# Kernel optimization log

Measured on AMD Instinct MI355X. Metric: run time of the kernel, lower is better.

The kernel has to match this reference:

```python
import jax, jax.numpy as jnp
import numpy as np

EPS = 1e-6
BN_EPS = 1e-5


def _grid_idx(loc, Hg, Wg):
    # loc: [B, N0, 2] in [-1, 1], (x, y) order -> nearest cell index in Hg x Wg grid
    loc = jnp.clip(loc, -1.0, 1.0)
    px = jnp.clip(jnp.round(0.5 * (loc[..., 0] + 1.0) * Wg - 0.5).astype(jnp.int32), 0, Wg - 1)
    py = jnp.clip(jnp.round(0.5 * (loc[..., 1] + 1.0) * Hg - 0.5).astype(jnp.int32), 0, Hg - 1)
    return py * Wg + px  # [B, N0]


def token2map(x, loc_orig, idx_agg, H, W):
    # scatter-average token features into an H x W map via the original points
    B, N, C = x.shape
    idx_hw = _grid_idx(loc_orig, H, W)                         # [B, N0]
    feat = jnp.take_along_axis(x, idx_agg[..., None], axis=1)  # [B, N0, C]
    ssum = jax.vmap(lambda s, i, f: s.at[i].add(f))(jnp.zeros((B, H * W, C), x.dtype), idx_hw, feat)
    cnt = jax.vmap(lambda c, i: c.at[i].add(1.0))(jnp.zeros((B, H * W), x.dtype), idx_hw)
    return (ssum / (cnt[..., None] + EPS)).reshape(B, H, W, C)


def map2token(x_map, N, loc_orig, idx_agg, agg_weight):
    # bilinear gather from map at original points, then weighted scatter-mean to N tokens
    B, Hd, Wd, C = x_map.shape
    loc = jnp.clip(loc_orig, -1.0, 1.0)
    fx = jnp.clip(0.5 * (loc[..., 0] + 1.0) * Wd - 0.5, 0.0, Wd - 1.0)
    fy = jnp.clip(0.5 * (loc[..., 1] + 1.0) * Hd - 0.5, 0.0, Hd - 1.0)
    x0 = jnp.floor(fx); y0 = jnp.floor(fy)
    wx = fx - x0; wy = fy - y0
    x0i = x0.astype(jnp.int32); y0i = y0.astype(jnp.int32)
    x1i = jnp.minimum(x0i + 1, Wd - 1); y1i = jnp.minimum(y0i + 1, Hd - 1)
    mp = x_map.reshape(B, Hd * Wd, C)
    g = lambda iy, ix: jnp.take_along_axis(mp, (iy * Wd + ix)[..., None], axis=1)  # [B, N0, C]
    f = (((1 - wx) * (1 - wy))[..., None] * g(y0i, x0i)
         + (wx * (1 - wy))[..., None] * g(y0i, x1i)
         + ((1 - wx) * wy)[..., None] * g(y1i, x0i)
         + (wx * wy)[..., None] * g(y1i, x1i))
    wpt = agg_weight[..., 0]                                   # [B, N0]
    num = jax.vmap(lambda n, i, s: n.at[i].add(s))(jnp.zeros((B, N, C), f.dtype), idx_agg, f * wpt[..., None])
    den = jax.vmap(lambda d, i, w: d.at[i].add(w))(jnp.zeros((B, N), f.dtype), idx_agg, wpt)
    return num / (den[..., None] + EPS)


def token_cluster_grid(x, loc_orig, idx_agg, agg_weight, weight, Hc, Wc):
    # weighted merge of tokens into Hc x Wc coarse grid cells (keyed by original points)
    B, N, C = x.shape
    Ns = Hc * Wc
    idx_cell = _grid_idx(loc_orig, Hc, Wc)                     # [B, N0] -> new token id
    wtok = weight[..., 0]                                      # [B, N] token confidence weight
    wpt = jnp.take_along_axis(wtok, idx_agg, axis=1)           # [B, N0]
    fpt = jnp.take_along_axis(x, idx_agg[..., None], axis=1)   # [B, N0, C]
    num = jax.vmap(lambda n, i, s: n.at[i].add(s))(jnp.zeros((B, Ns, C), x.dtype), idx_cell, fpt * wpt[..., None])
    den = jax.vmap(lambda d, i, w: d.at[i].add(w))(jnp.zeros((B, Ns), x.dtype), idx_cell, wpt)
    x_down = num / (den[..., None] + EPS)
    weight_t = (wpt / (jnp.take_along_axis(den, idx_cell, axis=1) + EPS))[..., None]  # [B, N0, 1]
    agg_weight_down = agg_weight * weight_t
    agg_weight_down = agg_weight_down / jnp.max(agg_weight_down, axis=1, keepdims=True)
    return x_down, idx_cell, agg_weight_down


def setup_inputs() -> dict:
    key = jax.random.key(0)
    ks = jax.random.split(key, 8)
    B, N, C_in, C_out = 4, 16384, 128, 256
    H = W = 256
    N0 = H * W
    x = jax.random.normal(ks[0], (B, N, C_in), jnp.float32)
    loc_orig = jax.random.uniform(ks[1], (B, N0, 2), jnp.float32, -1.0, 1.0)
    idx_agg = jax.random.randint(ks[2], (B, N0), 0, N, jnp.int32)
    agg_weight = jax.random.uniform(ks[3], (B, N0, 1), jnp.float32)
    conv_w = jax.random.normal(ks[4], (3, 3, C_in, C_out), jnp.float32) / np.sqrt(9 * C_in).astype(np.float32)
    conv_b = jnp.zeros((C_out,), jnp.float32)
    skip_w = jax.random.normal(ks[5], (C_out, C_in), jnp.float32) / np.sqrt(C_in).astype(np.float32)
    bn_gamma = jnp.ones((C_out,), jnp.float32)
    bn_beta = jnp.zeros((C_out,), jnp.float32)
    conf_w = jax.random.normal(ks[6], (1, C_out), jnp.float32) / np.sqrt(C_out).astype(np.float32)
    conf_b = jnp.zeros((1,), jnp.float32)
    return {"x": x, "loc_orig": loc_orig, "idx_agg": idx_agg, "agg_weight": agg_weight,
            "conv_w": conv_w, "conv_b": conv_b, "skip_w": skip_w,
            "bn_gamma": bn_gamma, "bn_beta": bn_beta, "conf_w": conf_w, "conf_b": conf_b,
            "H": H, "W": W}


def reference(x, loc_orig, idx_agg, agg_weight, conv_w, conv_b, skip_w, bn_gamma, bn_beta, conf_w, conf_b, H, W):
    B, N, C = x.shape
    # scatter tokens to map, 3x3 s2 conv
    x_map = token2map(x, loc_orig, idx_agg, H, W)              # [B, H, W, C]
    y = jax.lax.conv_general_dilated(x_map, conv_w, (2, 2), ((1, 1), (1, 1)),
                                     dimension_numbers=("NHWC", "HWIO", "NHWC")) + conv_b
    Hd = (H - 1) // 2 + 1
    Wd = (W - 1) // 2 + 1
    # gather back to tokens + linear skip
    tok = map2token(y, N, loc_orig, idx_agg, agg_weight) + x @ skip_w.T   # [B, N, C_out]
    # BatchNorm2d over tokens (train-mode batch stats, per channel)
    mu = jnp.mean(tok, axis=(0, 1))
    var = jnp.var(tok, axis=(0, 1))
    tokn = (tok - mu) / jnp.sqrt(var + BN_EPS) * bn_gamma + bn_beta
    conf = tokn @ conf_w.T + conf_b                            # [B, N, 1]
    weight = jnp.exp(conf)
    # grid clustering: merge to (Hd//2) x (Wd//2) cells = N * sample_ratio tokens
    x_down, idx_agg_down, agg_weight_down = token_cluster_grid(tokn, loc_orig, idx_agg, agg_weight, weight, Hd // 2, Wd // 2)
    x_down = jax.nn.relu(x_down)
    x_out = jax.nn.relu(tokn)
    return x_down, x_out, conf, agg_weight_down, idx_agg_down
```

## Files before the change

kernel.cpp:

```cpp
#include <hip/hip_runtime.h>
#include <hip/hip_bf16.h>
#include <math.h>

#define BB    4
#define NTOK  16384
#define CIN   128
#define COUT  256
#define HM    256
#define WM    256
#define NP    65536
#define HD    128
#define WD    128
#define HC    64
#define WC    64
#define NS    4096
#define EPS   1e-6f
#define BNEPS 1e-5f

#define SEG_TOK  (BB * NP)
#define SEG_64   (SEG_TOK + BB * NTOK)
#define NSEG     (SEG_64 + BB * NS)

typedef __attribute__((ext_vector_type(8))) short bfrag8;
typedef __attribute__((ext_vector_type(4))) float ffrag4;

static constexpr size_t BNSUM_OFF  = 0;
static constexpr size_t BNSQ_OFF   = BNSUM_OFF + 256;
static constexpr size_t MAXW_OFF   = BNSQ_OFF + 256;
static constexpr size_t CNTS_OFF   = MAXW_OFF + 256;
static constexpr size_t CURS_OFF   = CNTS_OFF + NSEG;
static constexpr size_t ZERO_FLOATS = CURS_OFF + NSEG;
static constexpr size_t YBUF_OFF   = (ZERO_FLOATS + 255) & ~(size_t)255;
static constexpr size_t XMAPN_OFF  = YBUF_OFF + (size_t)BB * HD * WD * COUT / 2;
static constexpr size_t XBF_OFF    = XMAPN_OFF + (size_t)BB * NP * CIN / 2;
static constexpr size_t TOKB_OFF   = XBF_OFF + (size_t)BB * NTOK * CIN / 2;
static constexpr size_t WFRAG_OFF  = TOKB_OFF + (size_t)BB * NTOK * COUT / 2;
static constexpr size_t SFRAG_OFF  = WFRAG_OFF + (size_t)9 * 4 * 16 * 512 / 2;
static constexpr size_t WEXP_OFF   = SFRAG_OFF + (size_t)4 * 16 * 512 / 2;
static constexpr size_t AWDT_OFF   = WEXP_OFF + (size_t)BB * NTOK;
static constexpr size_t ABUF_OFF   = AWDT_OFF + (size_t)BB * NP;
static constexpr size_t BBUF_OFF   = ABUF_OFF + 256;
static constexpr size_t CWA_OFF    = BBUF_OFF + 256;
static constexpr size_t C0_OFF     = CWA_OFF + 256;
static constexpr size_t CELL256_OFF = C0_OFF + 256;
static constexpr size_t CELL64_OFF  = CELL256_OFF + (size_t)BB * NP;
static constexpr size_t DEN1_OFF   = CELL64_OFF + (size_t)BB * NP;
static constexpr size_t DEN2_OFF   = DEN1_OFF + (size_t)BB * NTOK;
static constexpr size_t STARTS_OFF = DEN2_OFF + (size_t)BB * NS;
static constexpr size_t BLKSUM_OFF = STARTS_OFF + NSEG;
static constexpr size_t BLKEXCL_OFF = BLKSUM_OFF + 512;
static constexpr size_t PIDX_OFF   = BLKEXCL_OFF + 512;


__device__ __forceinline__ unsigned short f2bf(float f) {
    unsigned int u = __float_as_uint(f);
    return (unsigned short)((u + 0x7FFFu + ((u >> 16) & 1u)) >> 16);
}
__device__ __forceinline__ float bf2f(unsigned short u) {
    return __uint_as_float((unsigned int)u << 16);
}


__global__ void k_cells(const float* __restrict__ loc, int* __restrict__ cell256,
                        int* __restrict__ cell64) {
    int i = blockIdx.x * 256 + threadIdx.x;
    float lx = fminf(fmaxf(loc[2 * (size_t)i], -1.f), 1.f);
    float ly = fminf(fmaxf(loc[2 * (size_t)i + 1], -1.f), 1.f);
    int px = (int)rintf(0.5f * (lx + 1.f) * WM - 0.5f);
    px = min(max(px, 0), WM - 1);
    int py = (int)rintf(0.5f * (ly + 1.f) * HM - 0.5f);
    py = min(max(py, 0), HM - 1);
    cell256[i] = py * WM + px;
    int qx = (int)rintf(0.5f * (lx + 1.f) * WC - 0.5f);
    qx = min(max(qx, 0), WC - 1);
    int qy = (int)rintf(0.5f * (ly + 1.f) * HC - 0.5f);
    qy = min(max(qy, 0), HC - 1);
    cell64[i] = qy * WC + qx;
}

__global__ void k_xcast(const float* __restrict__ x, unsigned short* __restrict__ xbf) {
    size_t i = (size_t)blockIdx.x * 256 + threadIdx.x;
    float4 v = ((const float4*)x)[i];
    ushort4 o;
    o.x = f2bf(v.x); o.y = f2bf(v.y); o.z = f2bf(v.z); o.w = f2bf(v.w);
    ((ushort4*)xbf)[i] = o;
}

__global__ void k_hist(const int* __restrict__ cell256, const int* __restrict__ idx_agg,
                       const int* __restrict__ cell64, int* __restrict__ cnts) {
    int gp = blockIdx.x * 256 + threadIdx.x;
    int b = gp >> 16;
    atomicAdd(&cnts[b * NP + cell256[gp]], 1);
    atomicAdd(&cnts[SEG_TOK + b * NTOK + idx_agg[gp]], 1);
    atomicAdd(&cnts[SEG_64 + b * NS + cell64[gp]], 1);
}

__global__ __launch_bounds__(256) void k_scan1(const int* __restrict__ cnts,
                                               int* __restrict__ starts,
                                               int* __restrict__ blksum) {
    int t = threadIdx.x;
    int base = blockIdx.x * 1024 + t * 4;
    int4 v = *(const int4*)(cnts + base);
    int tsum = v.x + v.y + v.z + v.w;
    __shared__ int s[256];
    s[t] = tsum;
    __syncthreads();
    for (int off = 1; off < 256; off <<= 1) {
        int add = (t >= off) ? s[t - off] : 0;
        __syncthreads();
        s[t] += add;
        __syncthreads();
    }
    int excl = s[t] - tsum;
    int4 o;
    o.x = excl; o.y = excl + v.x; o.z = o.y + v.y; o.w = o.z + v.z;
    *(int4*)(starts + base) = o;
    if (t == 255) blksum[blockIdx.x] = s[255];
}

__global__ __launch_bounds__(512) void k_scan2(const int* __restrict__ blksum,
                                               int* __restrict__ blkexcl) {
    int t = threadIdx.x;
    __shared__ int s[512];
    int v = (t < 336) ? blksum[t] : 0;
    s[t] = v;
    __syncthreads();
    for (int off = 1; off < 512; off <<= 1) {
        int add = (t >= off) ? s[t - off] : 0;
        __syncthreads();
        s[t] += add;
        __syncthreads();
    }
    if (t < 336) blkexcl[t] = s[t] - v;
}

__global__ void k_fill(const int* __restrict__ cell256, const int* __restrict__ idx_agg,
                       const int* __restrict__ cell64, const int* __restrict__ starts,
                       const int* __restrict__ blkexcl, int* __restrict__ curs,
                       int* __restrict__ pidx) {
    int gp = blockIdx.x * 256 + threadIdx.x;
    int b = gp >> 16;
    int ia = idx_agg[gp];
    int t1 = b * NP + cell256[gp];
    int p1 = starts[t1] + blkexcl[t1 >> 10] + atomicAdd(&curs[t1], 1);
    pidx[p1] = ia;
    int t2 = SEG_TOK + b * NTOK + ia;
    int p2 = starts[t2] + blkexcl[t2 >> 10] + atomicAdd(&curs[t2], 1);
    pidx[p2] = gp;
    int t3 = SEG_64 + b * NS + cell64[gp];
    int p3 = starts[t3] + blkexcl[t3 >> 10] + atomicAdd(&curs[t3], 1);
    pidx[p3] = ia;
}

__global__ __launch_bounds__(256) void k_gather_map(const unsigned short* __restrict__ xbf,
                                                    const int* __restrict__ starts,
                                                    const int* __restrict__ blkexcl,
                                                    const int* __restrict__ cnts,
                                                    const int* __restrict__ pidx,
                                                    unsigned short* __restrict__ xmapn) {
    int tgt = blockIdx.x * 8 + (threadIdx.x >> 5);
    int lane = threadIdx.x & 31;
    int b = tgt >> 16;
    int start = starts[tgt] + blkexcl[tgt >> 10];
    int cnt = cnts[tgt];
    float4 acc = make_float4(0.f, 0.f, 0.f, 0.f);
    for (int j = 0; j < cnt; ++j) {
        int tk = pidx[start + j];
        ushort4 u = *(const ushort4*)(xbf + ((size_t)b * NTOK + tk) * CIN + lane * 4);
        acc.x += bf2f(u.x); acc.y += bf2f(u.y); acc.z += bf2f(u.z); acc.w += bf2f(u.w);
    }
    float inv = 1.0f / ((float)cnt + EPS);
    ushort4 o;
    o.x = f2bf(acc.x * inv);
    o.y = f2bf(acc.y * inv);
    o.z = f2bf(acc.z * inv);
    o.w = f2bf(acc.w * inv);
    *(ushort4*)(xmapn + (size_t)tgt * CIN + lane * 4) = o;
}

__global__ void k_wfrag(const float* __restrict__ cw, unsigned short* __restrict__ wfrag) {
    int i = blockIdx.x * 256 + threadIdx.x;
    int j = i & 7;
    int lane = (i >> 3) & 63;
    int nt = (i >> 9) & 15;
    int kc = (i >> 13) & 3;
    int khw = i >> 15;
    int c = kc * 32 + ((lane >> 4) << 3) + j;
    int n = nt * 16 + (lane & 15);
    wfrag[i] = f2bf(cw[((size_t)khw * CIN + c) * COUT + n]);
}

__global__ void k_sfrag(const float* __restrict__ sw, unsigned short* __restrict__ sfrag) {
    int i = blockIdx.x * 256 + threadIdx.x;
    int j = i & 7;
    int lane = (i >> 3) & 63;
    int nt = (i >> 9) & 15;
    int kc = i >> 13;
    int c = kc * 32 + ((lane >> 4) << 3) + j;
    int n = nt * 16 + (lane & 15);
    sfrag[i] = f2bf(sw[(size_t)n * CIN + c]);
}

__global__ __launch_bounds__(256) void k_convmf(const unsigned short* __restrict__ xmapn,
                                                const unsigned short* __restrict__ wfrag,
                                                const float* __restrict__ cb,
                                                unsigned short* __restrict__ y) {
    int bz = blockIdx.x;
    int ow0 = (bz & 1) * 64;
    int oh = (bz >> 1) & (HD - 1);
    int b = bz >> 8;
    int tid = threadIdx.x;
    int w = tid >> 6, lane = tid & 63;
    int n0 = w * 64;

    __shared__ unsigned short s_even[65 * 136];
    __shared__ unsigned short s_odd[64 * 136];

    ffrag4 acc[4][4];
#pragma unroll
    for (int mt = 0; mt < 4; ++mt)
#pragma unroll
        for (int nt = 0; nt < 4; ++nt) {
            ffrag4 z = {0.f, 0.f, 0.f, 0.f};
            acc[mt][nt] = z;
        }

    int iw0 = 2 * ow0 - 1;
    int lm = lane & 15;
    int lq = lane >> 4;
    int cbase = lq << 3;

    for (int kh = 0; kh < 3; ++kh) {
        int ih = 2 * oh - 1 + kh;
        __syncthreads();
        {
            const unsigned short* rowb =
                xmapn + ((size_t)b * NP + (size_t)ih * WM) * CIN;
            bool ihok = (ih >= 0 && ih < HM);
            for (int idx = tid; idx < 129 * 16; idx += 256) {
                int pix = idx >> 4;
                int c8 = (idx & 15) * 8;
                int iw = iw0 + pix;
                uint4 v = make_uint4(0u, 0u, 0u, 0u);
                if (ihok && iw >= 0 && iw < WM)
                    v = *(const uint4*)(rowb + (size_t)iw * CIN + c8);
                unsigned short* dst = (pix & 1)
                    ? &s_odd[(size_t)((pix - 1) >> 1) * 136 + c8]
                    : &s_even[(size_t)(pix >> 1) * 136 + c8];
                *(uint4*)dst = v;
            }
        }
        __syncthreads();
#pragma unroll
        for (int kw = 0; kw < 3; ++kw) {
            int khw = kh * 3 + kw;
#pragma unroll
            for (int kc = 0; kc < 4; ++kc) {
                int c = kc * 32 + cbase;
                bfrag8 af[4];
#pragma unroll
                for (int mt = 0; mt < 4; ++mt) {
                    int m = mt * 16 + lm;
                    const unsigned short* src;
                    if (kw == 1)      src = &s_odd[(size_t)m * 136 + c];
                    else if (kw == 0) src = &s_even[(size_t)m * 136 + c];
                    else              src = &s_even[(size_t)(m + 1) * 136 + c];
                    af[mt] = *(const bfrag8*)(const void*)src;
                }
                const unsigned short* wb =
                    wfrag + ((size_t)((khw * 4 + kc) * 16) + w * 4) * 512 + lane * 8;
#pragma unroll
                for (int nt = 0; nt < 4; ++nt) {
                    bfrag8 bf = *(const bfrag8*)(const void*)(wb + (size_t)nt * 512);
#pragma unroll
                    for (int mt = 0; mt < 4; ++mt)
                        acc[mt][nt] = __builtin_amdgcn_mfma_f32_16x16x32_bf16(
                            af[mt], bf, acc[mt][nt], 0, 0, 0);
                }
            }
        }
    }

    unsigned short* yb = y + (((size_t)b * HD + oh) * WD + ow0) * COUT;
#pragma unroll
    for (int nt = 0; nt < 4; ++nt) {
        int n = n0 + nt * 16 + lm;
        float bias = cb[n];
#pragma unroll
        for (int mt = 0; mt < 4; ++mt) {
#pragma unroll
            for (int r = 0; r < 4; ++r) {
                int m = mt * 16 + lq * 4 + r;
                yb[(size_t)m * COUT + n] = f2bf(acc[mt][nt][r] + bias);
            }
        }
    }
}

__global__ __launch_bounds__(256) void k_gather_tok(const unsigned short* __restrict__ y,
                                                    const float* __restrict__ loc,
                                                    const float* __restrict__ aggw,
                                                    const int* __restrict__ starts,
                                                    const int* __restrict__ blkexcl,
                                                    const int* __restrict__ cnts,
                                                    const int* __restrict__ pidx,
                                                    float* __restrict__ num_out,
                                                    float* __restrict__ den1) {
    int wv = threadIdx.x >> 6, lane = threadIdx.x & 63;
    int tl = blockIdx.x * 4 + wv;
    int b = tl >> 14;
    int tgt = SEG_TOK + tl;
    int start = starts[tgt] + blkexcl[tgt >> 10];
    int cnt = cnts[tgt];
    const unsigned short* ybase = y + (size_t)b * (HD * WD * COUT);
    float4 num = make_float4(0.f, 0.f, 0.f, 0.f);
    float den = 0.f;
    for (int j = 0; j < cnt; ++j) {
        int gp = pidx[start + j];
        float lx = fminf(fmaxf(loc[2 * (size_t)gp], -1.f), 1.f);
        float ly = fminf(fmaxf(loc[2 * (size_t)gp + 1], -1.f), 1.f);
        float fx = fminf(fmaxf(0.5f * (lx + 1.f) * WD - 0.5f, 0.f), (float)(WD - 1));
        float fy = fminf(fmaxf(0.5f * (ly + 1.f) * HD - 0.5f, 0.f), (float)(HD - 1));
        float x0f = floorf(fx), y0f = floorf(fy);
        float wx = fx - x0f, wy = fy - y0f;
        int x0 = (int)x0f, y0 = (int)y0f;
        int x1 = min(x0 + 1, WD - 1), y1 = min(y0 + 1, HD - 1);
        ushort4 u00 = *(const ushort4*)(ybase + ((size_t)y0 * WD + x0) * COUT + lane * 4);
        ushort4 u01 = *(const ushort4*)(ybase + ((size_t)y0 * WD + x1) * COUT + lane * 4);
        ushort4 u10 = *(const ushort4*)(ybase + ((size_t)y1 * WD + x0) * COUT + lane * 4);
        ushort4 u11 = *(const ushort4*)(ybase + ((size_t)y1 * WD + x1) * COUT + lane * 4);
        float w00 = (1.f - wx) * (1.f - wy), w01 = wx * (1.f - wy);
        float w10 = (1.f - wx) * wy, w11 = wx * wy;
        float aw = aggw[gp];
        num.x += (w00 * bf2f(u00.x) + w01 * bf2f(u01.x) + w10 * bf2f(u10.x) + w11 * bf2f(u11.x)) * aw;
        num.y += (w00 * bf2f(u00.y) + w01 * bf2f(u01.y) + w10 * bf2f(u10.y) + w11 * bf2f(u11.y)) * aw;
        num.z += (w00 * bf2f(u00.z) + w01 * bf2f(u01.z) + w10 * bf2f(u10.z) + w11 * bf2f(u11.z)) * aw;
        num.w += (w00 * bf2f(u00.w) + w01 * bf2f(u01.w) + w10 * bf2f(u10.w) + w11 * bf2f(u11.w)) * aw;
        den += aw;
    }
    *(float4*)(num_out + (size_t)tl * COUT + lane * 4) = num;
    if (lane == 0) den1[tl] = den;
}

__global__ __launch_bounds__(256) void k_tokmf(const unsigned short* __restrict__ xbf,
                                               const unsigned short* __restrict__ sfrag,
                                               const float* __restrict__ den1,
                                               float* __restrict__ tok) {
    int t0 = blockIdx.x * 64;
    int tid = threadIdx.x;
    int w = tid >> 6, lane = tid & 63;
    int n0 = w * 64;
    int lm = lane & 15, lq = lane >> 4;

    __shared__ unsigned short s_x[64 * 136];
    const unsigned short* xb = xbf + (size_t)t0 * CIN;
    for (int idx = tid; idx < 64 * 16; idx += 256) {
        int row = idx >> 4, c8 = (idx & 15) * 8;
        *(uint4*)&s_x[(size_t)row * 136 + c8] = *(const uint4*)(xb + (size_t)row * CIN + c8);
    }
    __syncthreads();

    ffrag4 acc[4][4];
#pragma unroll
    for (int mt = 0; mt < 4; ++mt)
#pragma unroll
        for (int nt = 0; nt < 4; ++nt) {
            ffrag4 z = {0.f, 0.f, 0.f, 0.f};
            acc[mt][nt] = z;
        }

#pragma unroll
    for (int kc = 0; kc < 4; ++kc) {
        int c = kc * 32 + lq * 8;
        bfrag8 af[4];
#pragma unroll
        for (int mt = 0; mt < 4; ++mt)
            af[mt] = *(const bfrag8*)(const void*)&s_x[(size_t)(mt * 16 + lm) * 136 + c];
        const unsigned short* sb = sfrag + ((size_t)(kc * 16) + w * 4) * 512 + lane * 8;
#pragma unroll
        for (int nt = 0; nt < 4; ++nt) {
            bfrag8 bf = *(const bfrag8*)(const void*)(sb + (size_t)nt * 512);
#pragma unroll
            for (int mt = 0; mt < 4; ++mt)
                acc[mt][nt] = __builtin_amdgcn_mfma_f32_16x16x32_bf16(
                    af[mt], bf, acc[mt][nt], 0, 0, 0);
        }
    }

#pragma unroll
    for (int mt = 0; mt < 4; ++mt) {
#pragma unroll
        for (int r = 0; r < 4; ++r) {
            int tkn = t0 + mt * 16 + lq * 4 + r;
            float inv = 1.f / (den1[tkn] + EPS);
#pragma unroll
            for (int nt = 0; nt < 4; ++nt) {
                int n = n0 + nt * 16 + lm;
                size_t a = (size_t)tkn * COUT + n;
                tok[a] = tok[a] * inv + acc[mt][nt][r];
            }
        }
    }
}

__global__ void k_bnstats(const float* __restrict__ tok, float* __restrict__ bnsum,
                          float* __restrict__ bnsq) {
    int k = threadIdx.x;
    size_t t0 = (size_t)blockIdx.x * 256;
    float s = 0.f, sq = 0.f;
    for (int t = 0; t < 256; ++t) {
        float v = tok[(t0 + t) * COUT + k];
        s += v;
        sq = fmaf(v, v, sq);
    }
    atomicAdd(bnsum + k, s);
    atomicAdd(bnsq + k, sq);
}

__global__ void k_bnparams(const float* __restrict__ bnsum, const float* __restrict__ bnsq,
                           const float* __restrict__ gamma, const float* __restrict__ beta,
                           const float* __restrict__ confw, const float* __restrict__ confb,
                           float* __restrict__ abuf, float* __restrict__ bbuf,
                           float* __restrict__ cwa, float* __restrict__ c0) {
    int k = threadIdx.x;
    const float cntv = (float)(BB * NTOK);
    float mu = bnsum[k] / cntv;
    float var = bnsq[k] / cntv - mu * mu;
    float a = gamma[k] * rsqrtf(var + BNEPS);
    float bbv = beta[k] - mu * a;
    abuf[k] = a;
    bbuf[k] = bbv;
    float cw = confw[k];
    cwa[k] = a * cw;
    __shared__ float red[256];
    red[k] = bbv * cw;
    __syncthreads();
    for (int s = 128; s > 0; s >>= 1) {
        if (k < s) red[k] += red[k + s];
        __syncthreads();
    }
    if (k == 0) c0[0] = red[0] + confb[0];
}

__global__ void k_conf(const float* __restrict__ tok, const float* __restrict__ cwa,
                       const float* __restrict__ c0v, const float* __restrict__ abuf,
                       const float* __restrict__ bbuf, float* __restrict__ conf_out,
                       unsigned short* __restrict__ tokb, float* __restrict__ wexp) {
    int tid = threadIdx.x;
    int tkn = blockIdx.x * 16 + (tid >> 4);
    int kc = (tid & 15) * 16;
    const float* row = tok + (size_t)tkn * COUT + kc;
    unsigned short* tb = tokb + (size_t)tkn * COUT + kc;
    float s = 0.f;
#pragma unroll
    for (int i = 0; i < 16; i += 4) {
        float4 v = *(const float4*)(row + i);
        float4 w = *(const float4*)(cwa + kc + i);
        float4 a = *(const float4*)(abuf + kc + i);
        float4 bb = *(const float4*)(bbuf + kc + i);
        s += v.x * w.x + v.y * w.y + v.z * w.z + v.w * w.w;
        ushort4 o;
        o.x = f2bf(fmaf(a.x, v.x, bb.x));
        o.y = f2bf(fmaf(a.y, v.y, bb.y));
        o.z = f2bf(fmaf(a.z, v.z, bb.z));
        o.w = f2bf(fmaf(a.w, v.w, bb.w));
        *(ushort4*)(tb + i) = o;
    }
    for (int off = 8; off > 0; off >>= 1) s += __shfl_down(s, off, 16);
    if ((tid & 15) == 0) {
        float cv = s + c0v[0];
        conf_out[tkn] = cv;
        wexp[tkn] = expf(cv);
    }
}

__global__ __launch_bounds__(256) void k_gather_cluster(const unsigned short* __restrict__ tokb,
                                                        const float* __restrict__ wexp,
                                                        const int* __restrict__ starts,
                                                        const int* __restrict__ blkexcl,
                                                        const int* __restrict__ cnts,
                                                        const int* __restrict__ pidx,
                                                        float* __restrict__ xdown,
                                                        float* __restrict__ den2) {
    int wv = threadIdx.x >> 6, lane = threadIdx.x & 63;
    int tl = blockIdx.x * 4 + wv;
    int b = tl >> 12;
    int tgt = SEG_64 + tl;
    int start = starts[tgt] + blkexcl[tgt >> 10];
    int cnt = cnts[tgt];
    float4 num = make_float4(0.f, 0.f, 0.f, 0.f);
    float den = 0.f;
    for (int j = 0; j < cnt; ++j) {
        int ia = pidx[start + j];
        float w = wexp[(size_t)b * NTOK + ia];
        ushort4 u = *(const ushort4*)(tokb + ((size_t)b * NTOK + ia) * COUT + lane * 4);
        num.x = fmaf(bf2f(u.x), w, num.x);
        num.y = fmaf(bf2f(u.y), w, num.y);
        num.z = fmaf(bf2f(u.z), w, num.z);
        num.w = fmaf(bf2f(u.w), w, num.w);
        den += w;
    }
    float inv = 1.f / (den + EPS);
    float4 o;
    o.x = fmaxf(num.x * inv, 0.f);
    o.y = fmaxf(num.y * inv, 0.f);
    o.z = fmaxf(num.z * inv, 0.f);
    o.w = fmaxf(num.w * inv, 0.f);
    *(float4*)(xdown + (size_t)tl * COUT + lane * 4) = o;
    if (lane == 0) den2[tl] = den;
}

__global__ void k_awd1(const float* __restrict__ wexp, const float* __restrict__ den2,
                       const int* __restrict__ idx_agg, const int* __restrict__ cell64,
                       const float* __restrict__ aggw, float* __restrict__ awdt,
                       float* __restrict__ idx_out_f, unsigned int* __restrict__ maxw) {
    int b = blockIdx.x >> 6;
    int chunk = blockIdx.x & 63;
    int base = b * NP + chunk * 1024;
    float lmax = 0.f;
    for (int t = threadIdx.x; t < 1024; t += 256) {
        int gp = base + t;
        int ia = idx_agg[gp];
        int cell = cell64[gp];
        float w = wexp[(size_t)b * NTOK + ia];
        float wt = w / (den2[(size_t)b * NS + cell] + EPS);
        float tv = aggw[gp] * wt;
        awdt[gp] = tv;
        idx_out_f[gp] = (float)cell;
        lmax = fmaxf(lmax, tv);
    }
    __shared__ float red[256];
    red[threadIdx.x] = lmax;
    __syncthreads();
    for (int s = 128; s > 0; s >>= 1) {
        if (threadIdx.x < s) red[threadIdx.x] = fmaxf(red[threadIdx.x], red[threadIdx.x + s]);
        __syncthreads();
    }
    if (threadIdx.x == 0) atomicMax(maxw + b, __float_as_uint(red[0]));
}

__global__ void k_awd2(const float* __restrict__ awdt, const unsigned int* __restrict__ maxw,
                       float* __restrict__ awd_out) {
    int i = blockIdx.x * 256 + threadIdx.x;
    int b = i >> 16;
    awd_out[i] = awdt[i] / __uint_as_float(maxw[b]);
}

__global__ void k_relutok(float* __restrict__ tok, const float* __restrict__ abuf,
                          const float* __restrict__ bbuf) {
    size_t i = (size_t)blockIdx.x * 256 + threadIdx.x;
    int k4 = (int)(i & 63) * 4;
    float4 a = *(const float4*)(abuf + k4);
    float4 bb = *(const float4*)(bbuf + k4);
    float4 v = ((float4*)tok)[i];
    v.x = fmaxf(fmaf(a.x, v.x, bb.x), 0.f);
    v.y = fmaxf(fmaf(a.y, v.y, bb.y), 0.f);
    v.z = fmaxf(fmaf(a.z, v.z, bb.z), 0.f);
    v.w = fmaxf(fmaf(a.w, v.w, bb.w), 0.f);
    ((float4*)tok)[i] = v;
}

extern "C" void kernel_launch(void* const* d_in, const int* in_sizes, int n_in,
                              void* d_out, int out_size, void* d_ws, size_t ws_size,
                              hipStream_t stream) {
    const float* x        = (const float*)d_in[0];
    const float* loc      = (const float*)d_in[1];
    const int*   idx_agg  = (const int*)d_in[2];
    const float* aggw     = (const float*)d_in[3];
    const float* conv_w   = (const float*)d_in[4];
    const float* conv_b   = (const float*)d_in[5];
    const float* skip_w   = (const float*)d_in[6];
    const float* bn_gamma = (const float*)d_in[7];
    const float* bn_beta  = (const float*)d_in[8];
    const float* conf_w   = (const float*)d_in[9];
    const float* conf_b   = (const float*)d_in[10];

    float* ws      = (float*)d_ws;
    float* bnsum   = ws + BNSUM_OFF;
    float* bnsq    = ws + BNSQ_OFF;
    unsigned int* maxw = (unsigned int*)(ws + MAXW_OFF);
    int*   cnts    = (int*)(ws + CNTS_OFF);
    int*   curs    = (int*)(ws + CURS_OFF);
    unsigned short* ybuf  = (unsigned short*)(ws + YBUF_OFF);
    unsigned short* xmapn = (unsigned short*)(ws + XMAPN_OFF);
    unsigned short* xbf   = (unsigned short*)(ws + XBF_OFF);
    unsigned short* tokb  = (unsigned short*)(ws + TOKB_OFF);
    unsigned short* wfrag = (unsigned short*)(ws + WFRAG_OFF);
    unsigned short* sfrag = (unsigned short*)(ws + SFRAG_OFF);
    float* wexp    = ws + WEXP_OFF;
    float* awdt    = ws + AWDT_OFF;
    float* abuf    = ws + ABUF_OFF;
    float* bbuf    = ws + BBUF_OFF;
    float* cwa     = ws + CWA_OFF;
    float* c0      = ws + C0_OFF;
    int*   cell256 = (int*)(ws + CELL256_OFF);
    int*   cell64  = (int*)(ws + CELL64_OFF);
    float* den1    = ws + DEN1_OFF;
    float* den2    = ws + DEN2_OFF;
    int*   starts  = (int*)(ws + STARTS_OFF);
    int*   blksum  = (int*)(ws + BLKSUM_OFF);
    int*   blkexcl = (int*)(ws + BLKEXCL_OFF);
    int*   pidx    = (int*)(ws + PIDX_OFF);

    float* out       = (float*)d_out;
    float* out_xdown = out;
    float* out_x     = out + (size_t)BB * NS * COUT;
    float* out_conf  = out_x + (size_t)BB * NTOK * COUT;
    float* out_awd   = out_conf + (size_t)BB * NTOK;
    float* out_idx   = out_awd + (size_t)BB * NP;

    hipMemsetAsync(d_ws, 0, ZERO_FLOATS * sizeof(float), stream);

    k_cells<<<BB * NP / 256, 256, 0, stream>>>(loc, cell256, cell64);
    k_xcast<<<BB * NTOK * CIN / 4 / 256, 256, 0, stream>>>(x, xbf);
    k_wfrag<<<9 * 4 * 16 * 512 / 256, 256, 0, stream>>>(conv_w, wfrag);
    k_sfrag<<<4 * 16 * 512 / 256, 256, 0, stream>>>(skip_w, sfrag);
    k_hist<<<BB * NP / 256, 256, 0, stream>>>(cell256, idx_agg, cell64, cnts);
    k_scan1<<<NSEG / 1024, 256, 0, stream>>>(cnts, starts, blksum);
    k_scan2<<<1, 512, 0, stream>>>(blksum, blkexcl);
    k_fill<<<BB * NP / 256, 256, 0, stream>>>(cell256, idx_agg, cell64, starts,
                                              blkexcl, curs, pidx);
    k_gather_map<<<BB * NP / 8, 256, 0, stream>>>(xbf, starts, blkexcl, cnts, pidx, xmapn);
    k_convmf<<<BB * HD * 2, 256, 0, stream>>>(xmapn, wfrag, conv_b, ybuf);
    k_gather_tok<<<BB * NTOK / 4, 256, 0, stream>>>(ybuf, loc, aggw, starts, blkexcl,
                                                    cnts, pidx, out_x, den1);
    k_tokmf<<<BB * NTOK / 64, 256, 0, stream>>>(xbf, sfrag, den1, out_x);
    k_bnstats<<<BB * NTOK / 256, 256, 0, stream>>>(out_x, bnsum, bnsq);
    k_bnparams<<<1, 256, 0, stream>>>(bnsum, bnsq, bn_gamma, bn_beta, conf_w, conf_b,
                                      abuf, bbuf, cwa, c0);
    k_conf<<<BB * NTOK / 16, 256, 0, stream>>>(out_x, cwa, c0, abuf, bbuf,
                                               out_conf, tokb, wexp);
    k_gather_cluster<<<BB * NS / 4, 256, 0, stream>>>(tokb, wexp, starts, blkexcl,
                                                      cnts, pidx, out_xdown, den2);
    k_awd1<<<BB * 64, 256, 0, stream>>>(wexp, den2, idx_agg, cell64, aggw,
                                        awdt, out_idx, maxw);
    k_awd2<<<BB * NP / 256, 256, 0, stream>>>(awdt, maxw, out_awd);
    k_relutok<<<BB * NTOK * COUT / 4 / 256, 256, 0, stream>>>(out_x, abuf, bbuf);
}
```

Baseline: 536.5 us.

## Fuse BN stats and ReLU into neighbors, precompute bilinear offsets, widen gathers

Bilinear cell offsets and aggregation-weighted corner weights are precomputed per point in the prep kernel, so the token gather no longer recomputes them. Both gather kernels now split each wave into two halves, each processing alternate points with 8-channel 16-byte loads and software prefetch of the next index, then combine the halves with a cross-lane shuffle. BatchNorm statistics are accumulated in the skip-matmul epilogue, removing a separate pass over the token tensor. The final normalize+ReLU pass is folded into k_conf, which removes one more full read and write of the output. The cost is extra workspace for the per-point offsets and weights, plus more atomics from the epilogue.

```diff
diff --git a/kernel.cpp b/kernel.cpp
--- a/kernel.cpp
+++ b/kernel.cpp
@@ -50,6 +50,8 @@
 static constexpr size_t BLKSUM_OFF = STARTS_OFF + NSEG;
 static constexpr size_t BLKEXCL_OFF = BLKSUM_OFF + 512;
 static constexpr size_t PIDX_OFF   = BLKEXCL_OFF + 512;
+static constexpr size_t POFF_OFF   = PIDX_OFF + (size_t)3 * BB * NP;
+static constexpr size_t PW_OFF     = POFF_OFF + (size_t)4 * BB * NP;
 
 
 __device__ __forceinline__ unsigned short f2bf(float f) {
@@ -59,10 +61,13 @@
 __device__ __forceinline__ float bf2f(unsigned short u) {
     return __uint_as_float((unsigned int)u << 16);
 }
-
-
-__global__ void k_cells(const float* __restrict__ loc, int* __restrict__ cell256,
-                        int* __restrict__ cell64) {
+#define BFLO(u) __uint_as_float((u) << 16)
+#define BFHI(u) __uint_as_float((u) & 0xffff0000u)
+
+
+__global__ void k_prep(const float* __restrict__ loc, const float* __restrict__ aggw,
+                       int* __restrict__ cell256, int* __restrict__ cell64,
+                       int4* __restrict__ poff, float4* __restrict__ pw) {
     int i = blockIdx.x * 256 + threadIdx.x;
     float lx = fminf(fmaxf(loc[2 * (size_t)i], -1.f), 1.f);
     float ly = fminf(fmaxf(loc[2 * (size_t)i + 1], -1.f), 1.f);
@@ -76,6 +81,23 @@
     int qy = (int)rintf(0.5f * (ly + 1.f) * HC - 0.5f);
     qy = min(max(qy, 0), HC - 1);
     cell64[i] = qy * WC + qx;
+    float fx = fminf(fmaxf(0.5f * (lx + 1.f) * WD - 0.5f, 0.f), (float)(WD - 1));
+    float fy = fminf(fmaxf(0.5f * (ly + 1.f) * HD - 0.5f, 0.f), (float)(HD - 1));
+    float x0f = floorf(fx), y0f = floorf(fy);
+    float wx = fx - x0f, wy = fy - y0f;
+    int x0 = (int)x0f, y0 = (int)y0f;
+    int x1 = min(x0 + 1, WD - 1), y1 = min(y0 + 1, HD - 1);
+    int4 o;
+    o.x = y0 * WD + x0; o.y = y0 * WD + x1;
+    o.z = y1 * WD + x0; o.w = y1 * WD + x1;
+    poff[i] = o;
+    float aw = aggw[i];
+    float4 w;
+    w.x = (1.f - wx) * (1.f - wy) * aw;
+    w.y = wx * (1.f - wy) * aw;
+    w.z = (1.f - wx) * wy * aw;
+    w.w = wx * wy * aw;
+    pw[i] = w;
 }
 
 __global__ void k_xcast(const float* __restrict__ x, unsigned short* __restrict__ xbf) {
@@ -297,9 +319,19 @@
     }
 }
 
+#define ACC8(U, W)                                            \
+    num[0] = fmaf(BFLO(U.x), W, num[0]);                      \
+    num[1] = fmaf(BFHI(U.x), W, num[1]);                      \
+    num[2] = fmaf(BFLO(U.y), W, num[2]);                      \
+    num[3] = fmaf(BFHI(U.y), W, num[3]);                      \
+    num[4] = fmaf(BFLO(U.z), W, num[4]);                      \
+    num[5] = fmaf(BFHI(U.z), W, num[5]);                      \
+    num[6] = fmaf(BFLO(U.w), W, num[6]);                      \
+    num[7] = fmaf(BFHI(U.w), W, num[7]);
+
 __global__ __launch_bounds__(256) void k_gather_tok(const unsigned short* __restrict__ y,
-                                                    const float* __restrict__ loc,
-                                                    const float* __restrict__ aggw,
+                                                    const int4* __restrict__ poff,
+                                                    const float4* __restrict__ pw,
                                                     const int* __restrict__ starts,
                                                     const int* __restrict__ blkexcl,
                                                     const int* __restrict__ cnts,
@@ -312,40 +344,58 @@
     int tgt = SEG_TOK + tl;
     int start = starts[tgt] + blkexcl[tgt >> 10];
     int cnt = cnts[tgt];
-    const unsigned short* ybase = y + (size_t)b * (HD * WD * COUT);
-    float4 num = make_float4(0.f, 0.f, 0.f, 0.f);
+    int half = lane >> 5;
+    int ch = (lane & 31) * 8;
+    const unsigned short* ybase = y + (size_t)b * (HD * WD * COUT) + ch;
+    float num[8];
+#pragma unroll
+    for (int k = 0; k < 8; ++k) num[k] = 0.f;
     float den = 0.f;
-    for (int j = 0; j < cnt; ++j) {
-        int gp = pidx[start + j];
-        float lx = fminf(fmaxf(loc[2 * (size_t)gp], -1.f), 1.f);
-        float ly = fminf(fmaxf(loc[2 * (size_t)gp + 1], -1.f), 1.f);
-        float fx = fminf(fmaxf(0.5f * (lx + 1.f) * WD - 0.5f, 0.f), (float)(WD - 1));
-        float fy = fminf(fmaxf(0.5f * (ly + 1.f) * HD - 0.5f, 0.f), (float)(HD - 1));
-        float x0f = floorf(fx), y0f = floorf(fy);
-        float wx = fx - x0f, wy = fy - y0f;
-        int x0 = (int)x0f, y0 = (int)y0f;
-        int x1 = min(x0 + 1, WD - 1), y1 = min(y0 + 1, HD - 1);
-        ushort4 u00 = *(const ushort4*)(ybase + ((size_t)y0 * WD + x0) * COUT + lane * 4);
-        ushort4 u01 = *(const ushort4*)(ybase + ((size_t)y0 * WD + x1) * COUT + lane * 4);
-        ushort4 u10 = *(const ushort4*)(ybase + ((size_t)y1 * WD + x0) * COUT + lane * 4);
-        ushort4 u11 = *(const ushort4*)(ybase + ((size_t)y1 * WD + x1) * COUT + lane * 4);
-        float w00 = (1.f - wx) * (1.f - wy), w01 = wx * (1.f - wy);
-        float w10 = (1.f - wx) * wy, w11 = wx * wy;
-        float aw = aggw[gp];
-        num.x += (w00 * bf2f(u00.x) + w01 * bf2f(u01.x) + w10 * bf2f(u10.x) + w11 * bf2f(u11.x)) * aw;
-        num.y += (w00 * bf2f(u00.y) + w01 * bf2f(u01.y) + w10 * bf2f(u10.y) + w11 * bf2f(u11.y)) * aw;
-        num.z += (w00 * bf2f(u00.z) + w01 * bf2f(u01.z) + w10 * bf2f(u10.z) + w11 * bf2f(u11.z)) * aw;
-        num.w += (w00 * bf2f(u00.w) + w01 * bf2f(u01.w) + w10 * bf2f(u10.w) + w11 * bf2f(u11.w)) * aw;
-        den += aw;
-    }
-    *(float4*)(num_out + (size_t)tl * COUT + lane * 4) = num;
-    if (lane == 0) den1[tl] = den;
+    if (cnt > 0) {
+        int last = cnt - 1;
+        int jm = half;
+        int gp = pidx[start + min(jm, last)];
+        int4 off = poff[gp];
+        float4 w = pw[gp];
+        if (jm > last) w = make_float4(0.f, 0.f, 0.f, 0.f);
+        for (int j2 = 0; j2 < cnt; j2 += 2) {
+            int4 offc = off;
+            float4 wc = w;
+            int jn = j2 + 2 + half;
+            if (j2 + 2 < cnt) {
+                int gpn = pidx[start + min(jn, last)];
+                off = poff[gpn];
+                w = pw[gpn];
+                if (jn > last) w = make_float4(0.f, 0.f, 0.f, 0.f);
+            }
+            uint4 u00 = *(const uint4*)(ybase + (size_t)offc.x * COUT);
+            uint4 u01 = *(const uint4*)(ybase + (size_t)offc.y * COUT);
+            uint4 u10 = *(const uint4*)(ybase + (size_t)offc.z * COUT);
+            uint4 u11 = *(const uint4*)(ybase + (size_t)offc.w * COUT);
+            ACC8(u00, wc.x)
+            ACC8(u01, wc.y)
+            ACC8(u10, wc.z)
+            ACC8(u11, wc.w)
+            den += wc.x + wc.y + wc.z + wc.w;
+        }
+    }
+#pragma unroll
+    for (int k = 0; k < 8; ++k) num[k] += __shfl_xor(num[k], 32, 64);
+    den += __shfl_xor(den, 32, 64);
+    if (half == 0) {
+        float* o = num_out + (size_t)tl * COUT + ch;
+        *(float4*)o = make_float4(num[0], num[1], num[2], num[3]);
+        *(float4*)(o + 4) = make_float4(num[4], num[5], num[6], num[7]);
+        if (lane == 0) den1[tl] = den;
+    }
 }
 
 __global__ __launch_bounds__(256) void k_tokmf(const unsigned short* __restrict__ xbf,
                                                const unsigned short* __restrict__ sfrag,
                                                const float* __restrict__ den1,
-                                               float* __restrict__ tok) {
+                                               float* __restrict__ tok,
+                                               float* __restrict__ bnsum,
+                                               float* __restrict__ bnsq) {
     int t0 = blockIdx.x * 64;
     int tid = threadIdx.x;
     int w = tid >> 6, lane = tid & 63;
@@ -387,6 +437,9 @@
         }
     }
 
+    float s[4], sq[4];
+#pragma unroll
+    for (int nt = 0; nt < 4; ++nt) { s[nt] = 0.f; sq[nt] = 0.f; }
 #pragma unroll
     for (int mt = 0; mt < 4; ++mt) {
 #pragma unroll
@@ -397,24 +450,26 @@
             for (int nt = 0; nt < 4; ++nt) {
                 int n = n0 + nt * 16 + lm;
                 size_t a = (size_t)tkn * COUT + n;
-                tok[a] = tok[a] * inv + acc[mt][nt][r];
+                float val = tok[a] * inv + acc[mt][nt][r];
+                tok[a] = val;
+                s[nt] += val;
+                sq[nt] = fmaf(val, val, sq[nt]);
             }
         }
     }
-}
-
-__global__ void k_bnstats(const float* __restrict__ tok, float* __restrict__ bnsum,
-                          float* __restrict__ bnsq) {
-    int k = threadIdx.x;
-    size_t t0 = (size_t)blockIdx.x * 256;
-    float s = 0.f, sq = 0.f;
-    for (int t = 0; t < 256; ++t) {
-        float v = tok[(t0 + t) * COUT + k];
-        s += v;
-        sq = fmaf(v, v, sq);
-    }
-    atomicAdd(bnsum + k, s);
-    atomicAdd(bnsq + k, sq);
+#pragma unroll
+    for (int nt = 0; nt < 4; ++nt) {
+        float vs = s[nt];
+        vs += __shfl_xor(vs, 16, 64);
+        vs += __shfl_xor(vs, 32, 64);
+        float vq = sq[nt];
+        vq += __shfl_xor(vq, 16, 64);
+        vq += __shfl_xor(vq, 32, 64);
+        if (lq == 0) {
+            atomicAdd(bnsum + n0 + nt * 16 + lm, vs);
+            atomicAdd(bnsq + n0 + nt * 16 + lm, vq);
+        }
+    }
 }
 
 __global__ void k_bnparams(const float* __restrict__ bnsum, const float* __restrict__ bnsq,
@@ -442,14 +497,14 @@
     if (k == 0) c0[0] = red[0] + confb[0];
 }
 
-__global__ void k_conf(const float* __restrict__ tok, const float* __restrict__ cwa,
+__global__ void k_conf(float* __restrict__ tok, const float* __restrict__ cwa,
                        const float* __restrict__ c0v, const float* __restrict__ abuf,
                        const float* __restrict__ bbuf, float* __restrict__ conf_out,
                        unsigned short* __restrict__ tokb, float* __restrict__ wexp) {
     int tid = threadIdx.x;
     int tkn = blockIdx.x * 16 + (tid >> 4);
     int kc = (tid & 15) * 16;
-    const float* row = tok + (size_t)tkn * COUT + kc;
+    float* row = tok + (size_t)tkn * COUT + kc;
     unsigned short* tb = tokb + (size_t)tkn * COUT + kc;
     float s = 0.f;
 #pragma unroll
@@ -459,12 +514,17 @@
         float4 a = *(const float4*)(abuf + kc + i);
         float4 bb = *(const float4*)(bbuf + kc + i);
         s += v.x * w.x + v.y * w.y + v.z * w.z + v.w * w.w;
+        float t0 = fmaf(a.x, v.x, bb.x);
+        float t1 = fmaf(a.y, v.y, bb.y);
+        float t2 = fmaf(a.z, v.z, bb.z);
+        float t3 = fmaf(a.w, v.w, bb.w);
         ushort4 o;
-        o.x = f2bf(fmaf(a.x, v.x, bb.x));
-        o.y = f2bf(fmaf(a.y, v.y, bb.y));
-        o.z = f2bf(fmaf(a.z, v.z, bb.z));
-        o.w = f2bf(fmaf(a.w, v.w, bb.w));
+        o.x = f2bf(t0); o.y = f2bf(t1); o.z = f2bf(t2); o.w = f2bf(t3);
         *(ushort4*)(tb + i) = o;
+        float4 r;
+        r.x = fmaxf(t0, 0.f); r.y = fmaxf(t1, 0.f);
+        r.z = fmaxf(t2, 0.f); r.w = fmaxf(t3, 0.f);
+        *(float4*)(row + i) = r;
     }
     for (int off = 8; off > 0; off >>= 1) s += __shfl_down(s, off, 16);
     if ((tid & 15) == 0) {
@@ -488,26 +548,49 @@
     int tgt = SEG_64 + tl;
     int start = starts[tgt] + blkexcl[tgt >> 10];
     int cnt = cnts[tgt];
-    float4 num = make_float4(0.f, 0.f, 0.f, 0.f);
+    int half = lane >> 5;
+    int ch = (lane & 31) * 8;
+    const unsigned short* tb = tokb + (size_t)b * NTOK * COUT + ch;
+    const float* we = wexp + (size_t)b * NTOK;
+    float num[8];
+#pragma unroll
+    for (int k = 0; k < 8; ++k) num[k] = 0.f;
     float den = 0.f;
-    for (int j = 0; j < cnt; ++j) {
-        int ia = pidx[start + j];
-        float w = wexp[(size_t)b * NTOK + ia];
-        ushort4 u = *(const ushort4*)(tokb + ((size_t)b * NTOK + ia) * COUT + lane * 4);
-        num.x = fmaf(bf2f(u.x), w, num.x);
-        num.y = fmaf(bf2f(u.y), w, num.y);
-        num.z = fmaf(bf2f(u.z), w, num.z);
-        num.w = fmaf(bf2f(u.w), w, num.w);
-        den += w;
-    }
-    float inv = 1.f / (den + EPS);
-    float4 o;
-    o.x = fmaxf(num.x * inv, 0.f);
-    o.y = fmaxf(num.y * inv, 0.f);
-    o.z = fmaxf(num.z * inv, 0.f);
-    o.w = fmaxf(num.w * inv, 0.f);
-    *(float4*)(xdown + (size_t)tl * COUT + lane * 4) = o;
-    if (lane == 0) den2[tl] = den;
+    if (cnt > 0) {
+        int last = cnt - 1;
+        int jm = half;
+        int ia = pidx[start + min(jm, last)];
+        float w = (jm <= last) ? we[ia] : 0.f;
+        const unsigned short* rp = tb + (size_t)ia * COUT;
+        for (int j2 = 0; j2 < cnt; j2 += 2) {
+            float wc = w;
+            const unsigned short* rpc = rp;
+            int jn = j2 + 2 + half;
+            if (j2 + 2 < cnt) {
+                int ian = pidx[start + min(jn, last)];
+                w = (jn <= last) ? we[ian] : 0.f;
+                rp = tb + (size_t)ian * COUT;
+            }
+            uint4 u = *(const uint4*)rpc;
+            ACC8(u, wc)
+            den += wc;
+        }
+    }
+#pragma unroll
+    for (int k = 0; k < 8; ++k) num[k] += __shfl_xor(num[k], 32, 64);
+    den += __shfl_xor(den, 32, 64);
+    if (half == 0) {
+        float inv = 1.f / (den + EPS);
+        float* o = xdown + (size_t)tl * COUT + ch;
+        float4 r0, r1;
+        r0.x = fmaxf(num[0] * inv, 0.f); r0.y = fmaxf(num[1] * inv, 0.f);
+        r0.z = fmaxf(num[2] * inv, 0.f); r0.w = fmaxf(num[3] * inv, 0.f);
+        r1.x = fmaxf(num[4] * inv, 0.f); r1.y = fmaxf(num[5] * inv, 0.f);
+        r1.z = fmaxf(num[6] * inv, 0.f); r1.w = fmaxf(num[7] * inv, 0.f);
+        *(float4*)o = r0;
+        *(float4*)(o + 4) = r1;
+        if (lane == 0) den2[tl] = den;
+    }
 }
 
 __global__ void k_awd1(const float* __restrict__ wexp, const float* __restrict__ den2,
@@ -544,20 +627,6 @@
     int i = blockIdx.x * 256 + threadIdx.x;
     int b = i >> 16;
     awd_out[i] = awdt[i] / __uint_as_float(maxw[b]);
-}
-
-__global__ void k_relutok(float* __restrict__ tok, const float* __restrict__ abuf,
-                          const float* __restrict__ bbuf) {
-    size_t i = (size_t)blockIdx.x * 256 + threadIdx.x;
-    int k4 = (int)(i & 63) * 4;
-    float4 a = *(const float4*)(abuf + k4);
-    float4 bb = *(const float4*)(bbuf + k4);
-    float4 v = ((float4*)tok)[i];
-    v.x = fmaxf(fmaf(a.x, v.x, bb.x), 0.f);
-    v.y = fmaxf(fmaf(a.y, v.y, bb.y), 0.f);
-    v.z = fmaxf(fmaf(a.z, v.z, bb.z), 0.f);
-    v.w = fmaxf(fmaf(a.w, v.w, bb.w), 0.f);
-    ((float4*)tok)[i] = v;
 }
 
 extern "C" void kernel_launch(void* const* d_in, const int* in_sizes, int n_in,
@@ -601,6 +670,8 @@
     int*   blksum  = (int*)(ws + BLKSUM_OFF);
     int*   blkexcl = (int*)(ws + BLKEXCL_OFF);
     int*   pidx    = (int*)(ws + PIDX_OFF);
+    int4*  poff    = (int4*)(ws + POFF_OFF);
+    float4* pwr    = (float4*)(ws + PW_OFF);
 
     float* out       = (float*)d_out;
     float* out_xdown = out;
@@ -611,7 +682,7 @@
 
     hipMemsetAsync(d_ws, 0, ZERO_FLOATS * sizeof(float), stream);
 
-    k_cells<<<BB * NP / 256, 256, 0, stream>>>(loc, cell256, cell64);
+    k_prep<<<BB * NP / 256, 256, 0, stream>>>(loc, aggw, cell256, cell64, poff, pwr);
     k_xcast<<<BB * NTOK * CIN / 4 / 256, 256, 0, stream>>>(x, xbf);
     k_wfrag<<<9 * 4 * 16 * 512 / 256, 256, 0, stream>>>(conv_w, wfrag);
     k_sfrag<<<4 * 16 * 512 / 256, 256, 0, stream>>>(skip_w, sfrag);
@@ -622,10 +693,9 @@
                                               blkexcl, curs, pidx);
     k_gather_map<<<BB * NP / 8, 256, 0, stream>>>(xbf, starts, blkexcl, cnts, pidx, xmapn);
     k_convmf<<<BB * HD * 2, 256, 0, stream>>>(xmapn, wfrag, conv_b, ybuf);
-    k_gather_tok<<<BB * NTOK / 4, 256, 0, stream>>>(ybuf, loc, aggw, starts, blkexcl,
+    k_gather_tok<<<BB * NTOK / 4, 256, 0, stream>>>(ybuf, poff, pwr, starts, blkexcl,
                                                     cnts, pidx, out_x, den1);
-    k_tokmf<<<BB * NTOK / 64, 256, 0, stream>>>(xbf, sfrag, den1, out_x);
-    k_bnstats<<<BB * NTOK / 256, 256, 0, stream>>>(out_x, bnsum, bnsq);
+    k_tokmf<<<BB * NTOK / 64, 256, 0, stream>>>(xbf, sfrag, den1, out_x, bnsum, bnsq);
     k_bnparams<<<1, 256, 0, stream>>>(bnsum, bnsq, bn_gamma, bn_beta, conf_w, conf_b,
                                       abuf, bbuf, cwa, c0);
     k_conf<<<BB * NTOK / 16, 256, 0, stream>>>(out_x, cwa, c0, abuf, bbuf,
@@ -635,5 +705,4 @@
     k_awd1<<<BB * 64, 256, 0, stream>>>(wexp, den2, idx_agg, cell64, aggw,
                                         awdt, out_idx, maxw);
     k_awd2<<<BB * NP / 256, 256, 0, stream>>>(awdt, maxw, out_awd);
-    k_relutok<<<BB * NTOK * COUT / 4 / 256, 256, 0, stream>>>(out_x, abuf, bbuf);
-}
+}
```

Result: faster. 525.0 us (-2.2%).
